# Performance work log

Measured on AMD Instinct MI355X. Metric: run time of the kernel, lower is better.

## Reference

```python
import jax, jax.numpy as jnp
import numpy as np

NHEAD = 16
EPS_L1 = 1e-12
LN_EPS = 1e-5


def _layernorm(x, g, b):
    mu = jnp.mean(x, axis=-1, keepdims=True)
    var = jnp.mean(jnp.square(x - mu), axis=-1, keepdims=True)
    return (x - mu) / jnp.sqrt(var + LN_EPS) * g + b


def setup_inputs() -> dict:
    key = jax.random.key(0)
    ks = jax.random.split(key, 16)
    S, B, E, P, F = 2048, 2, 1024, 64, 4096
    sc = lambda n: 1.0 / np.sqrt(n)
    return {
        "src": jax.random.normal(ks[0], (S, B, E), jnp.float32),
        "pos_embed": jax.random.normal(ks[1], (B, P, S), jnp.float32),
        "in_proj_w": jax.random.normal(ks[2], (3 * E, E), jnp.float32) * sc(E),
        "in_proj_b": jnp.zeros((3 * E,), jnp.float32),
        "out_w": jax.random.normal(ks[3], (E, E), jnp.float32) * sc(E),
        "out_b": jnp.zeros((E,), jnp.float32),
        "lin1_w": jax.random.normal(ks[4], (F, E), jnp.float32) * sc(E),
        "lin1_b": jnp.zeros((F,), jnp.float32),
        "lin2_w": jax.random.normal(ks[5], (E, F), jnp.float32) * sc(F),
        "lin2_b": jnp.zeros((E,), jnp.float32),
        "ln1_g": jnp.ones((E,), jnp.float32),
        "ln1_b": jnp.zeros((E,), jnp.float32),
        "ln2_g": jnp.ones((E,), jnp.float32),
        "ln2_b": jnp.zeros((E,), jnp.float32),
        "pos_w": jax.random.normal(ks[6], (P, P), jnp.float32) * sc(P),
        "pos_b": jnp.zeros((P,), jnp.float32),
    }


def reference(src, pos_embed, in_proj_w, in_proj_b, out_w, out_b,
              lin1_w, lin1_b, lin2_w, lin2_b,
              ln1_g, ln1_b, ln2_g, ln2_b, pos_w, pos_b):
    S, B, E = src.shape
    H = NHEAD
    Dh = E // H

    # --- custom positional-similarity kernel (cosine_similarity w/ L1 norm) ---
    pe = jnp.einsum('bps,qp->bqs', pos_embed, pos_w) + pos_b[None, :, None]  # learnable pos
    l1 = jnp.maximum(jnp.sum(jnp.abs(pe), axis=1, keepdims=True), EPS_L1)
    pe = pe / l1                                                # [B,P,S]
    pos_sim = jnp.einsum('bps,bpt->bst', pe, pe)                # [B,S,S]

    # --- manual multi-head self-attention ---
    qkv = src @ in_proj_w.T + in_proj_b                          # [S,B,3E]
    q, k, v = jnp.split(qkv, 3, axis=-1)
    q = q * (Dh ** -0.5)
    to_bhsd = lambda t: jnp.transpose(t.reshape(S, B, H, Dh), (1, 2, 0, 3))
    q, k, v = to_bhsd(q), to_bhsd(k), to_bhsd(v)                 # [B,H,S,Dh]
    scores = jnp.einsum('bhsd,bhtd->bhst', q, k) + pos_sim[:, None]
    attn = jax.nn.softmax(scores, axis=-1)                       # [B,H,S,S]
    ctx = jnp.einsum('bhst,bhtd->bhsd', attn, v)                 # [B,H,S,Dh]
    ctx = jnp.transpose(ctx, (2, 0, 1, 3)).reshape(S, B, E)
    attn_out = ctx @ out_w.T + out_b

    # --- residual + norm + FFN (post-norm, relu) ---
    x = _layernorm(src + attn_out, ln1_g, ln1_b)
    ff = jax.nn.relu(x @ lin1_w.T + lin1_b) @ lin2_w.T + lin2_b
    return _layernorm(x + ff, ln2_g, ln2_b)
```

## Files before the change

kernel.cpp:

```cpp
#include <hip/hip_runtime.h>
#include <hip/hip_bf16.h>
#include <math.h>

#define S_LEN 2048
#define BATCH 2
#define EMB   1024
#define NH    16
#define DH    64
#define E3    3072
#define FF    4096
#define PP    64

typedef __bf16 bf16x8 __attribute__((ext_vector_type(8)));
typedef float  floatx4 __attribute__((ext_vector_type(4)));

__device__ __forceinline__ void load_lds16(const void* g, void* l) {
  __builtin_amdgcn_global_load_lds(
      (const __attribute__((address_space(1))) void*)g,
      (__attribute__((address_space(3))) void*)l, 16, 0, 0);
}

__global__ __launch_bounds__(256) void cvt_kernel(
    const float* __restrict__ in, __hip_bfloat16* __restrict__ out, int n)
{
  int i = (blockIdx.x * 256 + threadIdx.x) * 8;
  if (i >= n) return;
  float4 a = *(const float4*)&in[i];
  float4 b = *(const float4*)&in[i + 4];
  __hip_bfloat16 t[8];
  t[0] = __float2bfloat16(a.x); t[1] = __float2bfloat16(a.y);
  t[2] = __float2bfloat16(a.z); t[3] = __float2bfloat16(a.w);
  t[4] = __float2bfloat16(b.x); t[5] = __float2bfloat16(b.y);
  t[6] = __float2bfloat16(b.z); t[7] = __float2bfloat16(b.w);
  *(float4*)&out[i] = *(float4*)t;
}

__global__ __launch_bounds__(64) void pe_kernel(
    const float* __restrict__ pos_embed, const float* __restrict__ pos_w,
    const float* __restrict__ pos_b, __hip_bfloat16* __restrict__ peT)
{
  __shared__ float pw[PP * PP];
  int tid = threadIdx.x;
  for (int i = 0; i < PP; ++i) pw[i * PP + tid] = pos_w[i * PP + tid];
  __syncthreads();
  int s = blockIdx.x * 64 + tid;
  int b = blockIdx.y;
  float acc[PP];
#pragma unroll
  for (int q = 0; q < PP; ++q) acc[q] = pos_b[q];
  for (int p = 0; p < PP; ++p) {
    float x = pos_embed[(size_t)(b * PP + p) * S_LEN + s];
#pragma unroll
    for (int q = 0; q < PP; ++q) acc[q] += pw[q * PP + p] * x;
  }
  float l1 = 0.f;
#pragma unroll
  for (int q = 0; q < PP; ++q) l1 += fabsf(acc[q]);
  float inv = 1.f / fmaxf(l1, 1e-12f);
  __hip_bfloat16 tmp[PP];
#pragma unroll
  for (int q = 0; q < PP; ++q) tmp[q] = __float2bfloat16(acc[q] * inv);
  float4* dst = (float4*)&peT[((size_t)b * S_LEN + s) * PP];
#pragma unroll
  for (int i = 0; i < 8; ++i) dst[i] = ((float4*)tmp)[i];
}

template <int WR, int WC>
__global__ __launch_bounds__(256) void gemm_bf16(
    const __hip_bfloat16* __restrict__ A, const __hip_bfloat16* __restrict__ W,
    const float* __restrict__ bias, float* __restrict__ Cf,
    __hip_bfloat16* __restrict__ Cb, int M, int N, int K, int relu, int qkscale,
    long strideA, long strideW, long strideC)
{
  constexpr int BM = 2 * WR * 16;
  constexpr int BN = 2 * WC * 16;
  __shared__ __bf16 As[BM * 64];
  __shared__ __bf16 Bs[BN * 64];
  A += (size_t)blockIdx.z * strideA;
  W += (size_t)blockIdx.z * strideW;
  int tid = threadIdx.x;
  int bm = blockIdx.y * BM;
  int bn = blockIdx.x * BN;
  int wave = tid >> 6, lane = tid & 63;
  int wm = (wave & 1) * (WR * 16), wn = (wave >> 1) * (WC * 16);
  int srow = tid >> 3, scb = tid & 7;
  int gcb = scb ^ (srow & 7);
  const __hip_bfloat16* Ap = A + (size_t)(bm + srow) * K + gcb * 8;
  const __hip_bfloat16* Wp = W + (size_t)(bn + srow) * K + gcb * 8;
  __bf16* AsBase = As + tid * 8;
  __bf16* BsBase = Bs + tid * 8;
  int r15 = lane & 15, quad = lane >> 4;

  floatx4 acc[WR * WC];
#pragma unroll
  for (int i = 0; i < WR * WC; ++i) acc[i] = (floatx4){0.f, 0.f, 0.f, 0.f};

  for (int k0 = 0; k0 < K; k0 += 64) {
    __syncthreads();
#pragma unroll
    for (int io = 0; io < BM / 32; ++io)
      load_lds16(Ap + (size_t)(32 * io) * K + k0, AsBase + io * 2048);
#pragma unroll
    for (int io = 0; io < BN / 32; ++io)
      load_lds16(Wp + (size_t)(32 * io) * K + k0, BsBase + io * 2048);
    __syncthreads();
#pragma unroll
    for (int kc = 0; kc < 2; ++kc) {
      bf16x8 af[WR], bfv[WC];
      int kb = kc * 4 + quad;
#pragma unroll
      for (int i = 0; i < WR; ++i) {
        int rowa = wm + i * 16 + r15;
        af[i] = *(const bf16x8*)&As[rowa * 64 + (kb ^ (rowa & 7)) * 8];
      }
#pragma unroll
      for (int j = 0; j < WC; ++j) {
        int rowb = wn + j * 16 + r15;
        bfv[j] = *(const bf16x8*)&Bs[rowb * 64 + (kb ^ (rowb & 7)) * 8];
      }
#pragma unroll
      for (int i = 0; i < WR; ++i)
#pragma unroll
        for (int j = 0; j < WC; ++j)
          acc[i * WC + j] = __builtin_amdgcn_mfma_f32_16x16x32_bf16(
              af[i], bfv[j], acc[i * WC + j], 0, 0, 0);
    }
  }
  int crow0 = bm + wm + quad * 4;
  int ccol0 = bn + wn + r15;
  float* CfB = Cf ? Cf + (size_t)blockIdx.z * strideC : nullptr;
  __hip_bfloat16* CbB = Cb ? Cb + (size_t)blockIdx.z * strideC : nullptr;
#pragma unroll
  for (int j = 0; j < WC; ++j) {
    int col = ccol0 + j * 16;
    float bv = bias ? bias[col] : 0.f;
    float scale = (qkscale && col < EMB) ? 0.125f : 1.f;
#pragma unroll
    for (int i = 0; i < WR; ++i) {
#pragma unroll
      for (int r = 0; r < 4; ++r) {
        int row = crow0 + i * 16 + r;
        float v = (acc[i * WC + j][r] + bv) * scale;
        if (relu) v = fmaxf(v, 0.f);
        if (CfB) CfB[(size_t)row * N + col] = v;
        if (CbB) CbB[(size_t)row * N + col] = __float2bfloat16(v);
      }
    }
  }
}

__global__ __launch_bounds__(256) void transpose_v(
    const __hip_bfloat16* __restrict__ qkv, __hip_bfloat16* __restrict__ vT)
{
  __shared__ __hip_bfloat16 tile[64][72];
  int c0 = blockIdx.x * 64, t0 = blockIdx.y * 64, b = blockIdx.z;
  int tid = threadIdx.x;
#pragma unroll
  for (int i = 0; i < 2; ++i) {
    int k = tid * 2 + i;
    int row = k >> 3, col = (k & 7) * 8;
    float4 v = *(const float4*)&qkv[((size_t)(t0 + row) * BATCH + b) * E3 + 2 * EMB + c0 + col];
    __hip_bfloat16 tmp[8];
    *(float4*)tmp = v;
#pragma unroll
    for (int j = 0; j < 8; ++j) tile[row][col + j] = tmp[j];
  }
  __syncthreads();
#pragma unroll
  for (int i = 0; i < 2; ++i) {
    int k = tid * 2 + i;
    int crow = k >> 3, tcol = (k & 7) * 8;
    __hip_bfloat16 tmp[8];
#pragma unroll
    for (int j = 0; j < 8; ++j) tmp[j] = tile[tcol + j][crow];
    *(float4*)&vT[((size_t)(b * EMB + c0 + crow)) * S_LEN + t0 + tcol] = *(float4*)tmp;
  }
}

__global__ __launch_bounds__(256) void attn_mfma(
    const __hip_bfloat16* __restrict__ qkv,
    const __hip_bfloat16* __restrict__ vT,
    const float* __restrict__ pos_sim,
    __hip_bfloat16* __restrict__ ctx)
{
  __shared__ __bf16 Ks[2][4096];
  __shared__ __bf16 Vs[2][4096];
  __shared__ __bf16 Ps[8192];
  int tid = threadIdx.x;
  int q0 = blockIdx.x * 128, h = blockIdx.y, b = blockIdx.z;
  int w = tid >> 6, lane = tid & 63, quad = lane >> 4, r15 = lane & 15;
  int srow = tid >> 3, scb = tid & 7;
  int x7 = r15 & 7;

  const __hip_bfloat16* kbase = qkv + EMB + (size_t)h * DH;
  const __hip_bfloat16* vbase = vT + ((size_t)b * EMB + h * DH) * S_LEN;

  bf16x8 qa[2][2];
#pragma unroll
  for (int qb = 0; qb < 2; ++qb)
#pragma unroll
    for (int kc = 0; kc < 2; ++kc)
      qa[qb][kc] = *(const bf16x8*)&qkv[
          ((size_t)(q0 + w * 32 + qb * 16 + r15) * BATCH + b) * E3 +
          h * DH + kc * 32 + quad * 8];

#pragma unroll
  for (int i = 0; i < 2; ++i) {
    int row = i * 32 + srow;
    int gcb = scb ^ (row & 7);
    load_lds16(kbase + ((size_t)row * BATCH + b) * E3 + gcb * 8,
               Ks[0] + i * 2048 + tid * 8);
    load_lds16(vbase + (size_t)row * S_LEN + gcb * 8,
               Vs[0] + i * 2048 + tid * 8);
  }
  __syncthreads();

  floatx4 of[2][4];
#pragma unroll
  for (int qb = 0; qb < 2; ++qb)
#pragma unroll
    for (int j = 0; j < 4; ++j) of[qb][j] = (floatx4){0.f, 0.f, 0.f, 0.f};
  float lp[2] = {0.f, 0.f};

  const float* psb[2];
#pragma unroll
  for (int qb = 0; qb < 2; ++qb)
    psb[qb] = pos_sim + ((size_t)(b * S_LEN + q0 + w * 32 + qb * 16 + r15)) * S_LEN
              + quad * 4;
  __bf16* pw0 = Ps + (w * 2 + 0) * 1024;
  __bf16* pw1 = Ps + (w * 2 + 1) * 1024;

  for (int kt = 0; kt < 32; ++kt) {
    int cur = kt & 1;
    int t0 = kt * 64;
    floatx4 sf[2][4];
#pragma unroll
    for (int qb = 0; qb < 2; ++qb)
#pragma unroll
      for (int j = 0; j < 4; ++j)
        sf[qb][j] = *(const floatx4*)(psb[qb] + t0 + j * 16);
    if (kt < 31) {
      int tn = t0 + 64;
      int nb = cur ^ 1;
#pragma unroll
      for (int i = 0; i < 2; ++i) {
        int row = i * 32 + srow;
        int gcb = scb ^ (row & 7);
        load_lds16(kbase + ((size_t)(tn + row) * BATCH + b) * E3 + gcb * 8,
                   Ks[nb] + i * 2048 + tid * 8);
        load_lds16(vbase + (size_t)row * S_LEN + tn + gcb * 8,
                   Vs[nb] + i * 2048 + tid * 8);
      }
    }

#pragma unroll
    for (int j = 0; j < 4; ++j) {
      int rowk = j * 16 + r15;
      bf16x8 kf0 = *(const bf16x8*)&Ks[cur][rowk * 64 + (quad ^ (rowk & 7)) * 8];
      bf16x8 kf1 = *(const bf16x8*)&Ks[cur][rowk * 64 + ((4 + quad) ^ (rowk & 7)) * 8];
#pragma unroll
      for (int qb = 0; qb < 2; ++qb) {
        sf[qb][j] = __builtin_amdgcn_mfma_f32_16x16x32_bf16(kf0, qa[qb][0], sf[qb][j], 0, 0, 0);
        sf[qb][j] = __builtin_amdgcn_mfma_f32_16x16x32_bf16(kf1, qa[qb][1], sf[qb][j], 0, 0, 0);
      }
    }

#pragma unroll
    for (int qb = 0; qb < 2; ++qb) {
      __bf16* pwq = qb ? pw1 : pw0;
#pragma unroll
      for (int j = 0; j < 4; ++j) {
        float e0 = __expf(fminf(sf[qb][j][0], 60.f));
        float e1 = __expf(fminf(sf[qb][j][1], 60.f));
        float e2 = __expf(fminf(sf[qb][j][2], 60.f));
        float e3 = __expf(fminf(sf[qb][j][3], 60.f));
        lp[qb] += (e0 + e1) + (e2 + e3);
        __hip_bfloat16 t4[4];
        t4[0] = __float2bfloat16(e0); t4[1] = __float2bfloat16(e1);
        t4[2] = __float2bfloat16(e2); t4[3] = __float2bfloat16(e3);
        int addr = r15 * 64 + (((j * 2 + (quad >> 1)) ^ x7) * 8) + (quad & 1) * 4;
        *(float2*)&pwq[addr] = *(float2*)t4;
      }
    }
    __asm__ volatile("s_waitcnt lgkmcnt(0)" ::: "memory");

    bf16x8 pb00 = *(const bf16x8*)&pw0[r15 * 64 + ((quad ^ x7) * 8)];
    bf16x8 pb01 = *(const bf16x8*)&pw0[r15 * 64 + (((4 + quad) ^ x7) * 8)];
    bf16x8 pb10 = *(const bf16x8*)&pw1[r15 * 64 + ((quad ^ x7) * 8)];
    bf16x8 pb11 = *(const bf16x8*)&pw1[r15 * 64 + (((4 + quad) ^ x7) * 8)];
#pragma unroll
    for (int jd = 0; jd < 4; ++jd) {
      int rowd = jd * 16 + r15;
      bf16x8 vb0 = *(const bf16x8*)&Vs[cur][rowd * 64 + (quad ^ (rowd & 7)) * 8];
      bf16x8 vb1 = *(const bf16x8*)&Vs[cur][rowd * 64 + ((4 + quad) ^ (rowd & 7)) * 8];
      of[0][jd] = __builtin_amdgcn_mfma_f32_16x16x32_bf16(vb0, pb00, of[0][jd], 0, 0, 0);
      of[0][jd] = __builtin_amdgcn_mfma_f32_16x16x32_bf16(vb1, pb01, of[0][jd], 0, 0, 0);
      of[1][jd] = __builtin_amdgcn_mfma_f32_16x16x32_bf16(vb0, pb10, of[1][jd], 0, 0, 0);
      of[1][jd] = __builtin_amdgcn_mfma_f32_16x16x32_bf16(vb1, pb11, of[1][jd], 0, 0, 0);
    }
    __syncthreads();
  }

#pragma unroll
  for (int qb = 0; qb < 2; ++qb) {
    float l = lp[qb];
    l += __shfl_xor(l, 16, 64);
    l += __shfl_xor(l, 32, 64);
    float inv = 1.f / l;
    size_t rbase = ((size_t)(q0 + w * 32 + qb * 16 + r15) * BATCH + b) * EMB + h * DH;
#pragma unroll
    for (int jd = 0; jd < 4; ++jd) {
      __hip_bfloat16 o4[4];
      o4[0] = __float2bfloat16(of[qb][jd][0] * inv);
      o4[1] = __float2bfloat16(of[qb][jd][1] * inv);
      o4[2] = __float2bfloat16(of[qb][jd][2] * inv);
      o4[3] = __float2bfloat16(of[qb][jd][3] * inv);
      *(float2*)&ctx[rbase + jd * 16 + quad * 4] = *(float2*)o4;
    }
  }
}

__global__ __launch_bounds__(256) void ln_kernel(
    const float* __restrict__ x1, const float* __restrict__ x2,
    const float* __restrict__ g, const float* __restrict__ bb,
    float* __restrict__ out, __hip_bfloat16* __restrict__ out_bf)
{
  int row = blockIdx.x;
  int tid = threadIdx.x;
  const float* p1 = x1 + (size_t)row * EMB;
  const float* p2 = x2 + (size_t)row * EMB;
  float4 v1 = *(const float4*)&p1[tid * 4];
  float4 v2 = *(const float4*)&p2[tid * 4];
  float x[4] = {v1.x + v2.x, v1.y + v2.y, v1.z + v2.z, v1.w + v2.w};
  float s = x[0] + x[1] + x[2] + x[3];
  float s2 = x[0] * x[0] + x[1] * x[1] + x[2] * x[2] + x[3] * x[3];
#pragma unroll
  for (int off = 32; off >= 1; off >>= 1) {
    s  += __shfl_xor(s, off, 64);
    s2 += __shfl_xor(s2, off, 64);
  }
  __shared__ float ws1[4], ws2[4];
  int wid = tid >> 6, lane = tid & 63;
  if (lane == 0) { ws1[wid] = s; ws2[wid] = s2; }
  __syncthreads();
  s  = ws1[0] + ws1[1] + ws1[2] + ws1[3];
  s2 = ws2[0] + ws2[1] + ws2[2] + ws2[3];
  float mean = s * (1.f / EMB);
  float var  = s2 * (1.f / EMB) - mean * mean;
  float inv  = rsqrtf(var + 1e-5f);
  float4 gv = *(const float4*)&g[tid * 4];
  float4 bv = *(const float4*)&bb[tid * 4];
  float4 o;
  o.x = (x[0] - mean) * inv * gv.x + bv.x;
  o.y = (x[1] - mean) * inv * gv.y + bv.y;
  o.z = (x[2] - mean) * inv * gv.z + bv.z;
  o.w = (x[3] - mean) * inv * gv.w + bv.w;
  *(float4*)&out[(size_t)row * EMB + tid * 4] = o;
  if (out_bf) {
    __hip_bfloat16 t[4];
    t[0] = __float2bfloat16(o.x); t[1] = __float2bfloat16(o.y);
    t[2] = __float2bfloat16(o.z); t[3] = __float2bfloat16(o.w);
    *(float2*)&out_bf[(size_t)row * EMB + tid * 4] = *(float2*)t;
  }
}

extern "C" void kernel_launch(void* const* d_in, const int* in_sizes, int n_in,
                              void* d_out, int out_size, void* d_ws, size_t ws_size,
                              hipStream_t stream)
{
  const float* src       = (const float*)d_in[0];
  const float* pos_embed = (const float*)d_in[1];
  const float* in_proj_w = (const float*)d_in[2];
  const float* in_proj_b = (const float*)d_in[3];
  const float* out_w     = (const float*)d_in[4];
  const float* out_b     = (const float*)d_in[5];
  const float* lin1_w    = (const float*)d_in[6];
  const float* lin1_b    = (const float*)d_in[7];
  const float* lin2_w    = (const float*)d_in[8];
  const float* lin2_b    = (const float*)d_in[9];
  const float* ln1_g     = (const float*)d_in[10];
  const float* ln1_b     = (const float*)d_in[11];
  const float* ln2_g     = (const float*)d_in[12];
  const float* ln2_b     = (const float*)d_in[13];
  const float* pos_w     = (const float*)d_in[14];
  const float* pos_b     = (const float*)d_in[15];
  float* out = (float*)d_out;
  float* ws  = (float*)d_ws;

  __hip_bfloat16* peT    = (__hip_bfloat16*)ws;
  float* pos_sim         = ws + 131072;
  __hip_bfloat16* qkv_bf = (__hip_bfloat16*)(ws + 8519680);
  __hip_bfloat16* vT_bf  = (__hip_bfloat16*)(ws + 14811136);
  __hip_bfloat16* src_bf = (__hip_bfloat16*)(ws + 16908288);
  __hip_bfloat16* inw_bf  = (__hip_bfloat16*)(ws + 19005440);
  __hip_bfloat16* outw_bf = (__hip_bfloat16*)(ws + 20578304);
  __hip_bfloat16* ctx_bf = (__hip_bfloat16*)(ws + 21102592);
  __hip_bfloat16* l1w_bf = (__hip_bfloat16*)(ws + 23199744);
  __hip_bfloat16* l2w_bf = (__hip_bfloat16*)(ws + 25296896);
  float* proj            = ws + 27394048;
  __hip_bfloat16* x_bf   = (__hip_bfloat16*)ws;
  float* xbuf            = ws + 2097152;
  __hip_bfloat16* h1_bf  = (__hip_bfloat16*)(ws + 6291456);

  const int M = S_LEN * BATCH;

  cvt_kernel<<<4194304 / 2048, 256, 0, stream>>>(src, src_bf, 4194304);
  cvt_kernel<<<3145728 / 2048, 256, 0, stream>>>(in_proj_w, inw_bf, 3145728);
  cvt_kernel<<<1048576 / 2048, 256, 0, stream>>>(out_w, outw_bf, 1048576);
  cvt_kernel<<<4194304 / 2048, 256, 0, stream>>>(lin1_w, l1w_bf, 4194304);
  cvt_kernel<<<4194304 / 2048, 256, 0, stream>>>(lin2_w, l2w_bf, 4194304);
  pe_kernel<<<dim3(S_LEN / 64, BATCH), 64, 0, stream>>>(pos_embed, pos_w, pos_b, peT);
  gemm_bf16<4, 4><<<dim3(2048 / 128, 2048 / 128, BATCH), 256, 0, stream>>>(
      peT, peT, nullptr, pos_sim, nullptr, 2048, 2048, 64, 0, 0,
      (long)2048 * 64, (long)2048 * 64, (long)2048 * 2048);
  gemm_bf16<4, 4><<<dim3(E3 / 128, M / 128, 1), 256, 0, stream>>>(
      src_bf, inw_bf, in_proj_b, nullptr, qkv_bf, M, E3, EMB, 0, 1, 0, 0, 0);
  transpose_v<<<dim3(EMB / 64, S_LEN / 64, BATCH), 256, 0, stream>>>(qkv_bf, vT_bf);
  attn_mfma<<<dim3(S_LEN / 128, NH, BATCH), 256, 0, stream>>>(
      qkv_bf, vT_bf, pos_sim, ctx_bf);
  gemm_bf16<2, 4><<<dim3(EMB / 128, M / 64, 1), 256, 0, stream>>>(
      ctx_bf, outw_bf, out_b, proj, nullptr, M, EMB, EMB, 0, 0, 0, 0, 0);
  ln_kernel<<<dim3(M), 256, 0, stream>>>(src, proj, ln1_g, ln1_b, xbuf, x_bf);
  gemm_bf16<4, 4><<<dim3(FF / 128, M / 128, 1), 256, 0, stream>>>(
      x_bf, l1w_bf, lin1_b, nullptr, h1_bf, M, FF, EMB, 1, 0, 0, 0, 0);
  gemm_bf16<2, 4><<<dim3(EMB / 128, M / 64, 1), 256, 0, stream>>>(
      h1_bf, l2w_bf, lin2_b, proj, nullptr, M, EMB, FF, 0, 0, 0, 0, 0);
  ln_kernel<<<dim3(M), 256, 0, stream>>>(xbuf, proj, ln2_g, ln2_b, out, nullptr);
}
```

Baseline: 451.2 us.

## Split attention over key halves with combine kernel; merge weight conversions

Attention now splits the key range into two halves across extra blocks (split-K style), doubling the grid from 512 to 1024 blocks. Each half writes unnormalized partial outputs and row sums, and a new combine kernel adds them, normalizes and writes ctx. The P tile in LDS is halved by processing one query block at a time, which may help occupancy. The five fp32-to-bf16 conversion launches are merged into one kernel. The cost is an extra launch, extra global traffic for the partials, and bf16 rounding of the unnormalized partial sums.

```diff
diff --git a/kernel.cpp b/kernel.cpp
--- a/kernel.cpp
+++ b/kernel.cpp
@@ -20,19 +20,30 @@
       (__attribute__((address_space(3))) void*)l, 16, 0, 0);
 }
 
-__global__ __launch_bounds__(256) void cvt_kernel(
-    const float* __restrict__ in, __hip_bfloat16* __restrict__ out, int n)
-{
-  int i = (blockIdx.x * 256 + threadIdx.x) * 8;
-  if (i >= n) return;
-  float4 a = *(const float4*)&in[i];
-  float4 b = *(const float4*)&in[i + 4];
+__global__ __launch_bounds__(256) void cvt5_kernel(
+    const float* __restrict__ a0, const float* __restrict__ a1,
+    const float* __restrict__ a2, const float* __restrict__ a3,
+    const float* __restrict__ a4,
+    __hip_bfloat16* __restrict__ b0, __hip_bfloat16* __restrict__ b1,
+    __hip_bfloat16* __restrict__ b2, __hip_bfloat16* __restrict__ b3,
+    __hip_bfloat16* __restrict__ b4)
+{
+  int gid = blockIdx.x;
+  const float* src; __hip_bfloat16* dst; int base;
+  if (gid < 2048)      { src = a0; dst = b0; base = gid; }
+  else if (gid < 3584) { src = a1; dst = b1; base = gid - 2048; }
+  else if (gid < 4096) { src = a2; dst = b2; base = gid - 3584; }
+  else if (gid < 6144) { src = a3; dst = b3; base = gid - 4096; }
+  else                 { src = a4; dst = b4; base = gid - 6144; }
+  int i = (base * 256 + threadIdx.x) * 8;
+  float4 a = *(const float4*)&src[i];
+  float4 b = *(const float4*)&src[i + 4];
   __hip_bfloat16 t[8];
   t[0] = __float2bfloat16(a.x); t[1] = __float2bfloat16(a.y);
   t[2] = __float2bfloat16(a.z); t[3] = __float2bfloat16(a.w);
   t[4] = __float2bfloat16(b.x); t[5] = __float2bfloat16(b.y);
   t[6] = __float2bfloat16(b.z); t[7] = __float2bfloat16(b.w);
-  *(float4*)&out[i] = *(float4*)t;
+  *(float4*)&dst[i] = *(float4*)t;
 }
 
 __global__ __launch_bounds__(64) void pe_kernel(
@@ -181,16 +192,19 @@
     const __hip_bfloat16* __restrict__ qkv,
     const __hip_bfloat16* __restrict__ vT,
     const float* __restrict__ pos_sim,
-    __hip_bfloat16* __restrict__ ctx)
+    __hip_bfloat16* __restrict__ opart,
+    float* __restrict__ lpart)
 {
   __shared__ __bf16 Ks[2][4096];
   __shared__ __bf16 Vs[2][4096];
-  __shared__ __bf16 Ps[8192];
+  __shared__ __bf16 Ps[4096];
   int tid = threadIdx.x;
-  int q0 = blockIdx.x * 128, h = blockIdx.y, b = blockIdx.z;
+  int q0 = blockIdx.x * 128, h = blockIdx.y;
+  int b = blockIdx.z & 1, half = blockIdx.z >> 1;
   int w = tid >> 6, lane = tid & 63, quad = lane >> 4, r15 = lane & 15;
   int srow = tid >> 3, scb = tid & 7;
   int x7 = r15 & 7;
+  int tbase = half * 1024;
 
   const __hip_bfloat16* kbase = qkv + EMB + (size_t)h * DH;
   const __hip_bfloat16* vbase = vT + ((size_t)b * EMB + h * DH) * S_LEN;
@@ -208,9 +222,9 @@
   for (int i = 0; i < 2; ++i) {
     int row = i * 32 + srow;
     int gcb = scb ^ (row & 7);
-    load_lds16(kbase + ((size_t)row * BATCH + b) * E3 + gcb * 8,
+    load_lds16(kbase + ((size_t)(tbase + row) * BATCH + b) * E3 + gcb * 8,
                Ks[0] + i * 2048 + tid * 8);
-    load_lds16(vbase + (size_t)row * S_LEN + gcb * 8,
+    load_lds16(vbase + (size_t)row * S_LEN + tbase + gcb * 8,
                Vs[0] + i * 2048 + tid * 8);
   }
   __syncthreads();
@@ -227,19 +241,18 @@
   for (int qb = 0; qb < 2; ++qb)
     psb[qb] = pos_sim + ((size_t)(b * S_LEN + q0 + w * 32 + qb * 16 + r15)) * S_LEN
               + quad * 4;
-  __bf16* pw0 = Ps + (w * 2 + 0) * 1024;
-  __bf16* pw1 = Ps + (w * 2 + 1) * 1024;
-
-  for (int kt = 0; kt < 32; ++kt) {
+  __bf16* pw = Ps + w * 1024;
+
+  for (int kt = 0; kt < 16; ++kt) {
     int cur = kt & 1;
-    int t0 = kt * 64;
+    int t0 = tbase + kt * 64;
     floatx4 sf[2][4];
 #pragma unroll
     for (int qb = 0; qb < 2; ++qb)
 #pragma unroll
       for (int j = 0; j < 4; ++j)
         sf[qb][j] = *(const floatx4*)(psb[qb] + t0 + j * 16);
-    if (kt < 31) {
+    if (kt < 15) {
       int tn = t0 + 64;
       int nb = cur ^ 1;
 #pragma unroll
@@ -267,7 +280,6 @@
 
 #pragma unroll
     for (int qb = 0; qb < 2; ++qb) {
-      __bf16* pwq = qb ? pw1 : pw0;
 #pragma unroll
       for (int j = 0; j < 4; ++j) {
         float e0 = __expf(fminf(sf[qb][j][0], 60.f));
@@ -279,24 +291,19 @@
         t4[0] = __float2bfloat16(e0); t4[1] = __float2bfloat16(e1);
         t4[2] = __float2bfloat16(e2); t4[3] = __float2bfloat16(e3);
         int addr = r15 * 64 + (((j * 2 + (quad >> 1)) ^ x7) * 8) + (quad & 1) * 4;
-        *(float2*)&pwq[addr] = *(float2*)t4;
-      }
-    }
-    __asm__ volatile("s_waitcnt lgkmcnt(0)" ::: "memory");
-
-    bf16x8 pb00 = *(const bf16x8*)&pw0[r15 * 64 + ((quad ^ x7) * 8)];
-    bf16x8 pb01 = *(const bf16x8*)&pw0[r15 * 64 + (((4 + quad) ^ x7) * 8)];
-    bf16x8 pb10 = *(const bf16x8*)&pw1[r15 * 64 + ((quad ^ x7) * 8)];
-    bf16x8 pb11 = *(const bf16x8*)&pw1[r15 * 64 + (((4 + quad) ^ x7) * 8)];
-#pragma unroll
-    for (int jd = 0; jd < 4; ++jd) {
-      int rowd = jd * 16 + r15;
-      bf16x8 vb0 = *(const bf16x8*)&Vs[cur][rowd * 64 + (quad ^ (rowd & 7)) * 8];
-      bf16x8 vb1 = *(const bf16x8*)&Vs[cur][rowd * 64 + ((4 + quad) ^ (rowd & 7)) * 8];
-      of[0][jd] = __builtin_amdgcn_mfma_f32_16x16x32_bf16(vb0, pb00, of[0][jd], 0, 0, 0);
-      of[0][jd] = __builtin_amdgcn_mfma_f32_16x16x32_bf16(vb1, pb01, of[0][jd], 0, 0, 0);
-      of[1][jd] = __builtin_amdgcn_mfma_f32_16x16x32_bf16(vb0, pb10, of[1][jd], 0, 0, 0);
-      of[1][jd] = __builtin_amdgcn_mfma_f32_16x16x32_bf16(vb1, pb11, of[1][jd], 0, 0, 0);
+        *(float2*)&pw[addr] = *(float2*)t4;
+      }
+      __asm__ volatile("s_waitcnt lgkmcnt(0)" ::: "memory");
+      bf16x8 pb0 = *(const bf16x8*)&pw[r15 * 64 + ((quad ^ x7) * 8)];
+      bf16x8 pb1 = *(const bf16x8*)&pw[r15 * 64 + (((4 + quad) ^ x7) * 8)];
+#pragma unroll
+      for (int jd = 0; jd < 4; ++jd) {
+        int rowd = jd * 16 + r15;
+        bf16x8 vb0 = *(const bf16x8*)&Vs[cur][rowd * 64 + (quad ^ (rowd & 7)) * 8];
+        bf16x8 vb1 = *(const bf16x8*)&Vs[cur][rowd * 64 + ((4 + quad) ^ (rowd & 7)) * 8];
+        of[qb][jd] = __builtin_amdgcn_mfma_f32_16x16x32_bf16(vb0, pb0, of[qb][jd], 0, 0, 0);
+        of[qb][jd] = __builtin_amdgcn_mfma_f32_16x16x32_bf16(vb1, pb1, of[qb][jd], 0, 0, 0);
+      }
     }
     __syncthreads();
   }
@@ -306,18 +313,40 @@
     float l = lp[qb];
     l += __shfl_xor(l, 16, 64);
     l += __shfl_xor(l, 32, 64);
-    float inv = 1.f / l;
-    size_t rbase = ((size_t)(q0 + w * 32 + qb * 16 + r15) * BATCH + b) * EMB + h * DH;
+    int qflat = (b * NH + h) * S_LEN + q0 + w * 32 + qb * 16 + r15;
+    if (quad == 0) lpart[half * (BATCH * NH * S_LEN) + qflat] = l;
+    __hip_bfloat16* obase =
+        opart + ((size_t)half * (BATCH * NH * S_LEN) + qflat) * DH;
 #pragma unroll
     for (int jd = 0; jd < 4; ++jd) {
       __hip_bfloat16 o4[4];
-      o4[0] = __float2bfloat16(of[qb][jd][0] * inv);
-      o4[1] = __float2bfloat16(of[qb][jd][1] * inv);
-      o4[2] = __float2bfloat16(of[qb][jd][2] * inv);
-      o4[3] = __float2bfloat16(of[qb][jd][3] * inv);
-      *(float2*)&ctx[rbase + jd * 16 + quad * 4] = *(float2*)o4;
-    }
-  }
+      o4[0] = __float2bfloat16(of[qb][jd][0]);
+      o4[1] = __float2bfloat16(of[qb][jd][1]);
+      o4[2] = __float2bfloat16(of[qb][jd][2]);
+      o4[3] = __float2bfloat16(of[qb][jd][3]);
+      *(float2*)&obase[jd * 16 + quad * 4] = *(float2*)o4;
+    }
+  }
+}
+
+__global__ __launch_bounds__(256) void attn_combine(
+    const __hip_bfloat16* __restrict__ opart, const float* __restrict__ lpart,
+    __hip_bfloat16* __restrict__ ctx)
+{
+  const int BHS = BATCH * NH * S_LEN;
+  int t = blockIdx.x * 256 + threadIdx.x;
+  int qf = t >> 3;
+  int dd = (t & 7) * 8;
+  float inv = 1.f / (lpart[qf] + lpart[BHS + qf]);
+  __hip_bfloat16 a[8], c[8], o[8];
+  *(float4*)a = *(const float4*)&opart[(size_t)qf * DH + dd];
+  *(float4*)c = *(const float4*)&opart[((size_t)BHS + qf) * DH + dd];
+#pragma unroll
+  for (int j = 0; j < 8; ++j)
+    o[j] = __float2bfloat16(
+        (__bfloat162float(a[j]) + __bfloat162float(c[j])) * inv);
+  int b = qf >> 15, h = (qf >> 11) & 15, q = qf & 2047;
+  *(float4*)&ctx[((size_t)(q * BATCH + b)) * EMB + h * DH + dd] = *(float4*)o;
 }
 
 __global__ __launch_bounds__(256) void ln_kernel(
@@ -398,17 +427,17 @@
   __hip_bfloat16* l1w_bf = (__hip_bfloat16*)(ws + 23199744);
   __hip_bfloat16* l2w_bf = (__hip_bfloat16*)(ws + 25296896);
   float* proj            = ws + 27394048;
+  __hip_bfloat16* opart  = (__hip_bfloat16*)(ws + 27394048);
+  float* lpart           = ws;
   __hip_bfloat16* x_bf   = (__hip_bfloat16*)ws;
   float* xbuf            = ws + 2097152;
   __hip_bfloat16* h1_bf  = (__hip_bfloat16*)(ws + 6291456);
 
   const int M = S_LEN * BATCH;
 
-  cvt_kernel<<<4194304 / 2048, 256, 0, stream>>>(src, src_bf, 4194304);
-  cvt_kernel<<<3145728 / 2048, 256, 0, stream>>>(in_proj_w, inw_bf, 3145728);
-  cvt_kernel<<<1048576 / 2048, 256, 0, stream>>>(out_w, outw_bf, 1048576);
-  cvt_kernel<<<4194304 / 2048, 256, 0, stream>>>(lin1_w, l1w_bf, 4194304);
-  cvt_kernel<<<4194304 / 2048, 256, 0, stream>>>(lin2_w, l2w_bf, 4194304);
+  cvt5_kernel<<<8192, 256, 0, stream>>>(
+      src, in_proj_w, out_w, lin1_w, lin2_w,
+      src_bf, inw_bf, outw_bf, l1w_bf, l2w_bf);
   pe_kernel<<<dim3(S_LEN / 64, BATCH), 64, 0, stream>>>(pos_embed, pos_w, pos_b, peT);
   gemm_bf16<4, 4><<<dim3(2048 / 128, 2048 / 128, BATCH), 256, 0, stream>>>(
       peT, peT, nullptr, pos_sim, nullptr, 2048, 2048, 64, 0, 0,
@@ -416,8 +445,10 @@
   gemm_bf16<4, 4><<<dim3(E3 / 128, M / 128, 1), 256, 0, stream>>>(
       src_bf, inw_bf, in_proj_b, nullptr, qkv_bf, M, E3, EMB, 0, 1, 0, 0, 0);
   transpose_v<<<dim3(EMB / 64, S_LEN / 64, BATCH), 256, 0, stream>>>(qkv_bf, vT_bf);
-  attn_mfma<<<dim3(S_LEN / 128, NH, BATCH), 256, 0, stream>>>(
-      qkv_bf, vT_bf, pos_sim, ctx_bf);
+  attn_mfma<<<dim3(S_LEN / 128, NH, 2 * BATCH), 256, 0, stream>>>(
+      qkv_bf, vT_bf, pos_sim, opart, lpart);
+  attn_combine<<<(BATCH * NH * S_LEN * (DH / 8)) / 256, 256, 0, stream>>>(
+      opart, lpart, ctx_bf);
   gemm_bf16<2, 4><<<dim3(EMB / 128, M / 64, 1), 256, 0, stream>>>(
       ctx_bf, outw_bf, out_b, proj, nullptr, M, EMB, EMB, 0, 0, 0, 0, 0);
   ln_kernel<<<dim3(M), 256, 0, stream>>>(src, proj, ln1_g, ln1_b, xbuf, x_bf);
```

Result: slower. 467.1 us (+3.5%).
